# Performance work log

Measured on AMD Instinct MI355X. Metric: run time of the kernel, lower is better.

The kernel has to match this reference:

```python
import jax, jax.numpy as jnp
import numpy as np

MIN_PERSISTENCE = [0.0, 0.0]  # from init kwargs, one per homology dimension


def setup_inputs() -> dict:
    key = jax.random.key(0)
    k1, k2, k3 = jax.random.split(key, 3)
    D = 512
    N = D * D * D  # 134,217,728 voxels
    P = 2_000_000  # persistence pairs per homology dimension
    X = jax.random.normal(k1, (D, D, D), dtype=jnp.float32)
    # Stand-ins for GUDHI cofaces_of_persistence_pairs() output:
    # flat (birth_idx, death_idx) pairs into Xflat, interleaved, per dimension.
    indices0 = jax.random.randint(k2, (2 * P,), 0, N, dtype=jnp.int32)
    indices1 = jax.random.randint(k3, (2 * P,), 0, N, dtype=jnp.int32)
    return {"X": X, "indices0": indices0, "indices1": indices1}


def _diagram(Xflat, indices, min_pers):
    # gather birth/death filtration values -> [num_pairs, 2]
    dgm = jnp.take(Xflat, indices).reshape(-1, 2)
    if min_pers >= 0:
        # Original uses tf.where + gather (dynamic shape). For jit we keep a
        # fixed shape and zero out points with persistence <= min_pers.
        keep = jnp.abs(dgm[:, 1] - dgm[:, 0]) > min_pers
        dgm = jnp.where(keep[:, None], dgm, jnp.zeros((), dgm.dtype))
    return dgm


def reference(X, indices0, indices1):
    Xflat = X.reshape(-1)
    dgm0 = _diagram(Xflat, indices0, MIN_PERSISTENCE[0])
    dgm1 = _diagram(Xflat, indices1, MIN_PERSISTENCE[1])
    return (dgm0, dgm1)
```

## Files before the change

### kernel.cpp

```cpp
#include <hip/hip_runtime.h>


typedef int   v4i __attribute__((ext_vector_type(4)));
typedef float v4f __attribute__((ext_vector_type(4)));

#define NCHUNK 8

__global__ __launch_bounds__(256) void warm_kernel(
    const v4f* __restrict__ Xc, int n16)
{
    int i = blockIdx.x * blockDim.x + threadIdx.x;
    float acc = 0.0f;
    if (i < n16) {
        v4f v = Xc[i];
        acc = v.x + v.y + v.z + v.w;
    }
    asm volatile("" :: "v"(acc));
}

__global__ __launch_bounds__(256) void gather_range_kernel(
    const float* __restrict__ X,
    const int* __restrict__ idx0,
    const int* __restrict__ idx1,
    float* __restrict__ out,
    int n4_0, int n4_total, int lo, int hi)
{
    constexpr int C = 4;
    const int tid    = blockIdx.x * blockDim.x + threadIdx.x;
    const int stride = gridDim.x * blockDim.x;

    int  c[C];
    v4i  ij[C];
    bool ok[C];
    #pragma unroll
    for (int j = 0; j < C; ++j) {
        c[j]  = tid + j * stride;
        ok[j] = c[j] < n4_total;
        int cc = ok[j] ? c[j] : 0;
        const v4i* p = (cc < n4_0)
            ? reinterpret_cast<const v4i*>(idx0) + cc
            : reinterpret_cast<const v4i*>(idx1) + (cc - n4_0);
        ij[j] = *p;
    }

    #pragma unroll
    for (int j = 0; j < C; ++j) {
        if (!ok[j]) continue;
        float* o = out + 4 * (size_t)c[j];
        #pragma unroll
        for (int k = 0; k < 4; ++k) {
            int id = (k == 0) ? ij[j].x : (k == 1) ? ij[j].y
                   : (k == 2) ? ij[j].z : ij[j].w;
            if (id >= lo && id < hi)
                o[k] = X[id];
        }
    }
}

__global__ __launch_bounds__(256) void pair_filter_kernel(
    float* __restrict__ out, int n4)
{
    int i = blockIdx.x * 256 + threadIdx.x;
    if (i >= n4) return;
    v4f* p = reinterpret_cast<v4f*>(out) + i;
    v4f o = *p;
    bool k0 = o.y != o.x;
    bool k1 = o.w != o.z;
    v4f r;
    r.x = k0 ? o.x : 0.0f;
    r.y = k0 ? o.y : 0.0f;
    r.z = k1 ? o.z : 0.0f;
    r.w = k1 ? o.w : 0.0f;
    *p = r;
}

__global__ __launch_bounds__(256) void gather_diagram_kernel(
    const float* __restrict__ X,
    const int* __restrict__ idx0,
    const int* __restrict__ idx1,
    float* __restrict__ out,
    int n4_0, int n4_total)
{
    constexpr int C = 4;
    const int tid    = blockIdx.x * blockDim.x + threadIdx.x;
    const int stride = gridDim.x * blockDim.x;

    int  c[C];
    v4i  ij[C];
    bool ok[C];
    #pragma unroll
    for (int j = 0; j < C; ++j) {
        c[j]  = tid + j * stride;
        ok[j] = c[j] < n4_total;
        int cc = ok[j] ? c[j] : 0;
        const v4i* p = (cc < n4_0)
            ? reinterpret_cast<const v4i*>(idx0) + cc
            : reinterpret_cast<const v4i*>(idx1) + (cc - n4_0);
        ij[j] = *p;
    }

    float v[C][4];
    #pragma unroll
    for (int j = 0; j < C; ++j) {
        v[j][0] = X[ij[j].x];
        v[j][1] = X[ij[j].y];
        v[j][2] = X[ij[j].z];
        v[j][3] = X[ij[j].w];
    }

    #pragma unroll
    for (int j = 0; j < C; ++j) {
        bool k0 = v[j][1] != v[j][0];
        bool k1 = v[j][3] != v[j][2];
        v4f o;
        o.x = k0 ? v[j][0] : 0.0f;
        o.y = k0 ? v[j][1] : 0.0f;
        o.z = k1 ? v[j][2] : 0.0f;
        o.w = k1 ? v[j][3] : 0.0f;
        if (ok[j]) {
            v4f* po = reinterpret_cast<v4f*>(out) + c[j];
            *po = o;
        }
    }
}

extern "C" void kernel_launch(void* const* d_in, const int* in_sizes, int n_in,
                              void* d_out, int out_size, void* d_ws, size_t ws_size,
                              hipStream_t stream) {
    const float* X        = (const float*)d_in[0];
    const int*   indices0 = (const int*)d_in[1];
    const int*   indices1 = (const int*)d_in[2];
    float*       out      = (float*)d_out;

    const int nX       = in_sizes[0];
    const int n0       = in_sizes[1];
    const int n1       = in_sizes[2];
    const int n4_0     = n0 / 4;
    const int n4_total = (n0 + n1) / 4;

    if ((n0 & 3) || (n1 & 3) || n4_total <= 0 || nX <= 0) {
        constexpr int C = 4, BLOCK = 256;
        const int threads_needed = (n4_total + C - 1) / C;
        const int blocks = (threads_needed + BLOCK - 1) / BLOCK;
        if (blocks > 0)
            gather_diagram_kernel<<<blocks, BLOCK, 0, stream>>>(
                X, indices0, indices1, out, n4_0, n4_total);
        return;
    }

    constexpr int C = 4, BLOCK = 256;
    const int threads_needed = (n4_total + C - 1) / C;
    const int gblocks = (threads_needed + BLOCK - 1) / BLOCK;

    const int chunk = (nX + NCHUNK - 1) / NCHUNK;
    for (int p = 0; p < NCHUNK; ++p) {
        const int lo = p * chunk;
        if (lo >= nX) break;
        const int hi = (lo + chunk < nX) ? (lo + chunk) : nX;
        const int n16 = (hi - lo) / 4;
        if (n16 > 0)
            warm_kernel<<<(n16 + BLOCK - 1) / BLOCK, BLOCK, 0, stream>>>(
                reinterpret_cast<const v4f*>(X + lo), n16);
        gather_range_kernel<<<gblocks, BLOCK, 0, stream>>>(
            X, indices0, indices1, out, n4_0, n4_total, lo, hi);
    }

    pair_filter_kernel<<<(n4_total + 255) / 256, 256, 0, stream>>>(out, n4_total);
}
```

Baseline: 932.5 us.

## Replace per-window kernel launches with one cooperative kernel using grid syncs

Folds the eight windowed gather launches, their cache-warming kernels and the final pair-filter pass into one cooperative kernel. It walks the same address windows in sequence, separated by grid-wide barriers. Each thread loads its indices once, keeps the gathered values in registers across windows, doubles the pairs handled per thread, and applies the persistence filter before a single vector store. This removes repeated index reads, partial scattered output writes, the extra filter pass and launch overhead. In exchange it drops the streaming warm-up of each window, so every window is now served by cold random accesses, and the whole grid must be co-resident to run.

```diff
diff --git a/kernel.cpp b/kernel.cpp
--- a/kernel.cpp
+++ b/kernel.cpp
@@ -1,31 +1,26 @@
 #include <hip/hip_runtime.h>
+#include <hip/hip_cooperative_groups.h>
+
+namespace cg = cooperative_groups;
 
 
 typedef int   v4i __attribute__((ext_vector_type(4)));
 typedef float v4f __attribute__((ext_vector_type(4)));
 
-#define NCHUNK 8
+#define NWIN        8
+#define COOP_BLOCKS_MAX 1024
+#define CCHUNK      8
 
-__global__ __launch_bounds__(256) void warm_kernel(
-    const v4f* __restrict__ Xc, int n16)
-{
-    int i = blockIdx.x * blockDim.x + threadIdx.x;
-    float acc = 0.0f;
-    if (i < n16) {
-        v4f v = Xc[i];
-        acc = v.x + v.y + v.z + v.w;
-    }
-    asm volatile("" :: "v"(acc));
-}
-
-__global__ __launch_bounds__(256) void gather_range_kernel(
+__global__ __launch_bounds__(256, 4) void gather_windows_coop(
     const float* __restrict__ X,
     const int* __restrict__ idx0,
     const int* __restrict__ idx1,
     float* __restrict__ out,
-    int n4_0, int n4_total, int lo, int hi)
+    int n4_0, int n4_total, int wchunk, int nX)
 {
-    constexpr int C = 4;
+    constexpr int C = CCHUNK;
+    cg::grid_group grid = cg::this_grid();
+
     const int tid    = blockIdx.x * blockDim.x + threadIdx.x;
     const int stride = gridDim.x * blockDim.x;
 
@@ -43,35 +38,43 @@
         ij[j] = *p;
     }
 
+    float v[C][4];
     #pragma unroll
     for (int j = 0; j < C; ++j) {
-        if (!ok[j]) continue;
-        float* o = out + 4 * (size_t)c[j];
+        v[j][0] = 0.0f; v[j][1] = 0.0f; v[j][2] = 0.0f; v[j][3] = 0.0f;
+    }
+
+    int lo = 0;
+    for (int w = 0; w < NWIN; ++w) {
+        int hi = lo + wchunk;
+        if (hi > nX) hi = nX;
+        const unsigned span = (unsigned)(hi - lo);
         #pragma unroll
-        for (int k = 0; k < 4; ++k) {
-            int id = (k == 0) ? ij[j].x : (k == 1) ? ij[j].y
-                   : (k == 2) ? ij[j].z : ij[j].w;
-            if (id >= lo && id < hi)
-                o[k] = X[id];
+        for (int j = 0; j < C; ++j) {
+            #pragma unroll
+            for (int k = 0; k < 4; ++k) {
+                int id = (k == 0) ? ij[j].x : (k == 1) ? ij[j].y
+                       : (k == 2) ? ij[j].z : ij[j].w;
+                if ((unsigned)(id - lo) < span)
+                    v[j][k] = X[id];
+            }
         }
+        lo = hi;
+        if (w != NWIN - 1) grid.sync();
     }
-}
 
-__global__ __launch_bounds__(256) void pair_filter_kernel(
-    float* __restrict__ out, int n4)
-{
-    int i = blockIdx.x * 256 + threadIdx.x;
-    if (i >= n4) return;
-    v4f* p = reinterpret_cast<v4f*>(out) + i;
-    v4f o = *p;
-    bool k0 = o.y != o.x;
-    bool k1 = o.w != o.z;
-    v4f r;
-    r.x = k0 ? o.x : 0.0f;
-    r.y = k0 ? o.y : 0.0f;
-    r.z = k1 ? o.z : 0.0f;
-    r.w = k1 ? o.w : 0.0f;
-    *p = r;
+    #pragma unroll
+    for (int j = 0; j < C; ++j) {
+        bool k0 = v[j][1] != v[j][0];
+        bool k1 = v[j][3] != v[j][2];
+        v4f o;
+        o.x = k0 ? v[j][0] : 0.0f;
+        o.y = k0 ? v[j][1] : 0.0f;
+        o.z = k1 ? v[j][2] : 0.0f;
+        o.w = k1 ? v[j][3] : 0.0f;
+        if (ok[j])
+            *(reinterpret_cast<v4f*>(out) + c[j]) = o;
+    }
 }
 
 __global__ __launch_bounds__(256) void gather_diagram_kernel(
@@ -117,11 +120,20 @@
         o.y = k0 ? v[j][1] : 0.0f;
         o.z = k1 ? v[j][2] : 0.0f;
         o.w = k1 ? v[j][3] : 0.0f;
-        if (ok[j]) {
-            v4f* po = reinterpret_cast<v4f*>(out) + c[j];
-            *po = o;
-        }
+        if (ok[j])
+            *(reinterpret_cast<v4f*>(out) + c[j]) = o;
     }
+}
+
+static void launch_direct(const float* X, const int* idx0, const int* idx1,
+                          float* out, int n4_0, int n4_total,
+                          hipStream_t stream) {
+    constexpr int C = 4, BLOCK = 256;
+    const int threads_needed = (n4_total + C - 1) / C;
+    const int blocks = (threads_needed + BLOCK - 1) / BLOCK;
+    if (blocks > 0)
+        gather_diagram_kernel<<<blocks, BLOCK, 0, stream>>>(
+            X, idx0, idx1, out, n4_0, n4_total);
 }
 
 extern "C" void kernel_launch(void* const* d_in, const int* in_sizes, int n_in,
@@ -139,31 +151,28 @@
     const int n4_total = (n0 + n1) / 4;
 
     if ((n0 & 3) || (n1 & 3) || n4_total <= 0 || nX <= 0) {
-        constexpr int C = 4, BLOCK = 256;
-        const int threads_needed = (n4_total + C - 1) / C;
-        const int blocks = (threads_needed + BLOCK - 1) / BLOCK;
-        if (blocks > 0)
-            gather_diagram_kernel<<<blocks, BLOCK, 0, stream>>>(
-                X, indices0, indices1, out, n4_0, n4_total);
+        launch_direct(X, indices0, indices1, out, n4_0, n4_total, stream);
         return;
     }
 
-    constexpr int C = 4, BLOCK = 256;
-    const int threads_needed = (n4_total + C - 1) / C;
-    const int gblocks = (threads_needed + BLOCK - 1) / BLOCK;
-
-    const int chunk = (nX + NCHUNK - 1) / NCHUNK;
-    for (int p = 0; p < NCHUNK; ++p) {
-        const int lo = p * chunk;
-        if (lo >= nX) break;
-        const int hi = (lo + chunk < nX) ? (lo + chunk) : nX;
-        const int n16 = (hi - lo) / 4;
-        if (n16 > 0)
-            warm_kernel<<<(n16 + BLOCK - 1) / BLOCK, BLOCK, 0, stream>>>(
-                reinterpret_cast<const v4f*>(X + lo), n16);
-        gather_range_kernel<<<gblocks, BLOCK, 0, stream>>>(
-            X, indices0, indices1, out, n4_0, n4_total, lo, hi);
+    constexpr int BLOCK = 256;
+    const int threads_needed = (n4_total + CCHUNK - 1) / CCHUNK;
+    int blocks = (threads_needed + BLOCK - 1) / BLOCK;
+    if (blocks > COOP_BLOCKS_MAX) {
+        launch_direct(X, indices0, indices1, out, n4_0, n4_total, stream);
+        return;
     }
 
-    pair_filter_kernel<<<(n4_total + 255) / 256, 256, 0, stream>>>(out, n4_total);
+    int wchunk = (nX + NWIN - 1) / NWIN;
+    void* args[] = {
+        (void*)&X, (void*)&indices0, (void*)&indices1, (void*)&out,
+        (void*)&n4_0, (void*)&n4_total, (void*)&wchunk, (void*)&nX
+    };
+    hipError_t err = hipLaunchCooperativeKernel(
+        (const void*)gather_windows_coop,
+        dim3(blocks), dim3(BLOCK), args, 0, stream);
+    if (err != hipSuccess) {
+        (void)hipGetLastError();
+        launch_direct(X, indices0, indices1, out, n4_0, n4_total, stream);
+    }
 }
```

After: 1.559 ms. 67.2% more time.
